# Performance work log

Measured on AMD Instinct MI355X. Metric: run time of the kernel, lower is better.

## Reference

```python
import jax, jax.numpy as jnp
import numpy as np

N_NODES = 8192
K = 64


def setup_inputs() -> dict:
    key = jax.random.key(0)
    k1, k2 = jax.random.split(key)
    A = jax.random.normal(k1, (N_NODES, N_NODES), dtype=jnp.float32)
    idx = jax.random.randint(k2, (N_NODES,), 0, N_NODES, dtype=jnp.int64)
    return {"A": A, "idx": idx}


def reference(A, idx):
    # adj = relu(A)
    adj = jax.nn.relu(A)
    # per-row top-k indices (dim=1), then scatter a 0/1 mask and multiply
    _, ind = jax.lax.top_k(adj, K)  # ind: [N, K]
    rows = jnp.arange(adj.shape[0], dtype=ind.dtype)[:, None]  # [N, 1]
    mask = jnp.zeros_like(adj).at[rows, ind].set(1.0)
    return adj * mask
```

## Files before the change

kernel.cpp:

```cpp
#include <hip/hip_runtime.h>
#include <stdint.h>


constexpr int N      = 8192;
constexpr int K      = 64;
constexpr int BLOCK  = 256;
constexpr int VPT    = N / BLOCK;
constexpr int V4     = VPT / 4;
constexpr int CAP    = 1536;
constexpr int EQ_CAP = 256;

__device__ __forceinline__ uint32_t wave_reduce_add(uint32_t x) {
    #pragma unroll
    for (int d = 32; d >= 1; d >>= 1) x += __shfl_down(x, d, 64);
    return x;
}

__device__ __forceinline__ void scan_pick(const uint32_t* hist256,
                                          uint32_t* s_prefix, uint32_t* s_k,
                                          int shift, int lane) {
    uint32_t k  = *s_k;
    uint32_t h0 = hist256[4 * lane + 0];
    uint32_t h1 = hist256[4 * lane + 1];
    uint32_t h2 = hist256[4 * lane + 2];
    uint32_t h3 = hist256[4 * lane + 3];
    uint32_t suf = h0 + h1 + h2 + h3;
    #pragma unroll
    for (int d = 1; d < 64; d <<= 1) {
        uint32_t o = __shfl_down(suf, d, 64);
        if (lane + d < 64) suf += o;
    }
    unsigned long long m = __ballot(suf >= k);
    int cl = 63 - __builtin_clzll(m);
    if (lane == cl) {
        uint32_t S0 = suf, S1 = S0 - h0, S2 = S1 - h1, S3 = S2 - h2;
        int b; uint32_t Sb, hb;
        if      (S3 >= k) { b = 3; Sb = S3; hb = h3; }
        else if (S2 >= k) { b = 2; Sb = S2; hb = h2; }
        else if (S1 >= k) { b = 1; Sb = S1; hb = h1; }
        else              { b = 0; Sb = S0; hb = h0; }
        *s_prefix |= (uint32_t)(4 * lane + b) << shift;
        *s_k = k - (Sb - hb);
    }
}

__global__ __launch_bounds__(BLOCK) void topk_row_kernel(
    const float* __restrict__ A, float* __restrict__ out)
{
    __shared__ uint32_t hist[4][256];
    __shared__ uint32_t list[CAP];
    __shared__ uint32_t s_eq[EQ_CAP];
    __shared__ uint32_t s_rb[4][5];
    __shared__ uint32_t s_rmax[4];
    __shared__ uint32_t s_prefix, s_k, s_cnt, s_listcnt, s_C, s_ecut, s_mode, s_max;

    const int tid  = threadIdx.x;
    const int wave = tid >> 6;
    const int lane = tid & 63;
    const int row  = blockIdx.x;

    const float4* rowp = reinterpret_cast<const float4*>(A + (size_t)row * N);
    float4*       outp = reinterpret_cast<float4*>(out + (size_t)row * N);

    uint32_t v[VPT];
    #pragma unroll
    for (int j = 0; j < V4; ++j) {
        float4 f = rowp[tid + j * BLOCK];
        v[4*j+0] = (f.x > 0.f) ? __float_as_uint(f.x) : 0u;
        v[4*j+1] = (f.y > 0.f) ? __float_as_uint(f.y) : 0u;
        v[4*j+2] = (f.z > 0.f) ? __float_as_uint(f.z) : 0u;
        v[4*j+3] = (f.w > 0.f) ? __float_as_uint(f.w) : 0u;
    }
    if (tid == 0) { s_listcnt = 0; s_cnt = 0; }

    uint32_t mx = 0;
    #pragma unroll
    for (int j = 0; j < VPT; ++j) mx = (v[j] > mx) ? v[j] : mx;
    #pragma unroll
    for (int d = 32; d >= 1; d >>= 1) {
        uint32_t o = __shfl_down(mx, d, 64);
        mx = (o > mx) ? o : mx;
    }
    if (lane == 0) s_rmax[wave] = mx;
    __syncthreads();
    if (tid == 0) {
        uint32_t m = s_rmax[0];
        m = (s_rmax[1] > m) ? s_rmax[1] : m;
        m = (s_rmax[2] > m) ? s_rmax[2] : m;
        m = (s_rmax[3] > m) ? s_rmax[3] : m;
        s_max = m;
    }
    __syncthreads();
    const uint32_t expM = s_max >> 23;

    uint32_t b0 = 0, b1 = 0, b2 = 0, b3 = 0, cpos = 0;
    #pragma unroll
    for (int j = 0; j < VPT; ++j) {
        uint32_t x = v[j];
        if (x != 0u) {
            uint32_t d = expM - (x >> 23);
            cpos += 1u;
            b0 += (d == 0u); b1 += (d == 1u); b2 += (d == 2u); b3 += (d == 3u);
        }
    }
    b0 = wave_reduce_add(b0); b1 = wave_reduce_add(b1);
    b2 = wave_reduce_add(b2); b3 = wave_reduce_add(b3);
    cpos = wave_reduce_add(cpos);
    if (lane == 0) {
        s_rb[wave][0] = b0; s_rb[wave][1] = b1; s_rb[wave][2] = b2;
        s_rb[wave][3] = b3; s_rb[wave][4] = cpos;
    }
    __syncthreads();
    if (tid == 0) {
        uint32_t B[5];
        #pragma unroll
        for (int c = 0; c < 5; ++c)
            B[c] = s_rb[0][c] + s_rb[1][c] + s_rb[2][c] + s_rb[3][c];
        if (B[4] < (uint32_t)K) {
            s_mode = 1;
        } else {
            s_mode = 0;
            uint32_t cum = 0; int jf = -1;
            #pragma unroll
            for (int j = 0; j < 4; ++j) {
                cum += B[j];
                if (jf < 0 && cum >= (uint32_t)K) jf = j;
            }
            if (jf >= 0) {
                uint32_t c2 = 0;
                for (int j = 0; j <= jf; ++j) c2 += B[j];
                s_C = c2; s_ecut = expM - (uint32_t)jf;
            } else {
                s_C = 0;
            }
        }
    }
    __syncthreads();

    if (s_mode == 1) {
        #pragma unroll
        for (int j = 0; j < V4; ++j) {
            float4 o;
            o.x = __uint_as_float(v[4*j+0]); o.y = __uint_as_float(v[4*j+1]);
            o.z = __uint_as_float(v[4*j+2]); o.w = __uint_as_float(v[4*j+3]);
            outp[tid + j * BLOCK] = o;
        }
        return;
    }

    if (s_C == 0) {
        uint32_t ecut = (expM > 7u) ? (expM - 7u) : 0u;
        for (;;) {
            __syncthreads();
            uint32_t lc = 0;
            #pragma unroll
            for (int j = 0; j < VPT; ++j)
                lc += (v[j] != 0u && (v[j] >> 23) >= ecut) ? 1u : 0u;
            lc = wave_reduce_add(lc);
            if (lane == 0) s_rb[wave][0] = lc;
            __syncthreads();
            if (tid == 0) {
                s_C = s_rb[0][0] + s_rb[1][0] + s_rb[2][0] + s_rb[3][0];
                s_ecut = ecut;
            }
            __syncthreads();
            if (s_C >= (uint32_t)K || ecut == 0u) break;
            ecut = (ecut > 4u) ? (ecut - 4u) : 0u;
        }
    }
    __syncthreads();
    const uint32_t C    = s_C;
    const uint32_t ecut = s_ecut;

    #pragma unroll
    for (int c = 0; c < 4; ++c) hist[c][tid] = 0;
    if (tid == 0) { s_prefix = 0; s_k = K; }
    __syncthreads();

    if (C <= (uint32_t)CAP) {
        uint32_t lc = 0;
        #pragma unroll
        for (int j = 0; j < VPT; ++j)
            lc += (v[j] != 0u && (v[j] >> 23) >= ecut) ? 1u : 0u;
        uint32_t incl = lc;
        #pragma unroll
        for (int d = 1; d < 64; d <<= 1) {
            uint32_t t = __shfl_up(incl, d, 64);
            if (lane >= d) incl += t;
        }
        uint32_t baseV = 0;
        if (lane == 63) baseV = atomicAdd(&s_listcnt, incl);
        uint32_t base = __shfl(baseV, 63, 64);
        uint32_t pos  = base + (incl - lc);
        #pragma unroll
        for (int j = 0; j < VPT; ++j) {
            uint32_t x = v[j];
            if (x != 0u && (x >> 23) >= ecut) list[pos++] = x;
        }
        __syncthreads();

        for (uint32_t i = tid; i < C; i += BLOCK)
            atomicAdd(&hist[wave][list[i] >> 24], 1u);
        __syncthreads();
        hist[0][tid] = hist[0][tid] + hist[1][tid] + hist[2][tid] + hist[3][tid];
        __syncthreads();
        if (wave == 0) scan_pick(hist[0], &s_prefix, &s_k, 24, lane);
        __syncthreads();

        for (int shift = 16; shift >= 0; shift -= 8) {
            const uint32_t prefix = s_prefix;
            #pragma unroll
            for (int c = 0; c < 4; ++c) hist[c][tid] = 0;
            __syncthreads();
            const uint32_t himask = 0xFFFFFFFFu << (shift + 8);
            for (uint32_t i = tid; i < C; i += BLOCK) {
                uint32_t x = list[i];
                if ((x & himask) == prefix)
                    atomicAdd(&hist[wave][(x >> shift) & 255u], 1u);
            }
            __syncthreads();
            hist[0][tid] = hist[0][tid] + hist[1][tid] + hist[2][tid] + hist[3][tid];
            __syncthreads();
            if (wave == 0) scan_pick(hist[0], &s_prefix, &s_k, shift, lane);
            __syncthreads();
        }
    } else {
        #pragma unroll
        for (int j = 0; j < VPT; ++j) {
            uint32_t x = v[j];
            if (x) atomicAdd(&hist[wave][x >> 24], 1u);
        }
        __syncthreads();
        hist[0][tid] = hist[0][tid] + hist[1][tid] + hist[2][tid] + hist[3][tid];
        __syncthreads();
        if (wave == 0) scan_pick(hist[0], &s_prefix, &s_k, 24, lane);
        __syncthreads();

        for (int shift = 16; shift >= 0; shift -= 8) {
            const uint32_t prefix = s_prefix;
            #pragma unroll
            for (int c = 0; c < 4; ++c) hist[c][tid] = 0;
            __syncthreads();
            const uint32_t himask = 0xFFFFFFFFu << (shift + 8);
            #pragma unroll
            for (int j = 0; j < VPT; ++j) {
                uint32_t x = v[j];
                if ((x & himask) == prefix)
                    atomicAdd(&hist[wave][(x >> shift) & 255u], 1u);
            }
            __syncthreads();
            hist[0][tid] = hist[0][tid] + hist[1][tid] + hist[2][tid] + hist[3][tid];
            __syncthreads();
            if (wave == 0) scan_pick(hist[0], &s_prefix, &s_k, shift, lane);
            __syncthreads();
        }
    }

    const uint32_t T    = s_prefix;
    const uint32_t need = s_k;
    const float    Tf   = __uint_as_float(T);

    #pragma unroll
    for (int j = 0; j < V4; ++j) {
        const int base = (tid + j * BLOCK) * 4;
        float4 o;
        float* oc = &o.x;
        #pragma unroll
        for (int c = 0; c < 4; ++c) {
            uint32_t x = v[4*j+c];
            float val = 0.f;
            if (x > T) {
                val = __uint_as_float(x);
            } else if (x == T) {
                uint32_t p = atomicAdd(&s_cnt, 1u);
                if (p < (uint32_t)EQ_CAP) s_eq[p] = (uint32_t)(base + c);
            }
            oc[c] = val;
        }
        outp[tid + j * BLOCK] = o;
    }
    __syncthreads();

    if (tid == 0) {
        uint32_t cnt = s_cnt < (uint32_t)EQ_CAP ? s_cnt : (uint32_t)EQ_CAP;
        for (uint32_t n = 0; n < need; ++n) {
            uint32_t best = 0xFFFFFFFFu, bi = 0;
            for (uint32_t i = 0; i < cnt; ++i)
                if (s_eq[i] < best) { best = s_eq[i]; bi = i; }
            if (best != 0xFFFFFFFFu) {
                s_eq[bi] = 0xFFFFFFFFu;
                out[(size_t)row * N + best] = Tf;
            }
        }
    }
}

extern "C" void kernel_launch(void* const* d_in, const int* in_sizes, int n_in,
                              void* d_out, int out_size, void* d_ws, size_t ws_size,
                              hipStream_t stream) {
    const float* A = (const float*)d_in[0];
    float* out = (float*)d_out;
    topk_row_kernel<<<N, BLOCK, 0, stream>>>(A, out);
}
```

Before: 442.6 us.

## Seed radix select from exponent window bitmasks and early-exit on unique bucket

Replaces the per-row exponent-window counting with per-thread bitmasks and packed popcount reductions. The selected bucket's bitmask is reused to build the candidate list, and the radix select starts from the known exponent prefix. The select loop exits early once the bucket holds a single element. Other changes: double-buffered per-wave histograms summed inside the scan instead of a separate merge pass, fewer redundant barriers, nontemporal output stores, and a block-parallel tie fallback when the tie list overflows. The aim is to cut synchronisation and histogram passes per row, at the cost of more complex control flow and some extra LDS.

```diff
diff --git a/kernel.cpp b/kernel.cpp
--- a/kernel.cpp
+++ b/kernel.cpp
@@ -1,6 +1,8 @@
 #include <hip/hip_runtime.h>
 #include <stdint.h>
 
+
+typedef float f32x4 __attribute__((ext_vector_type(4)));
 
 constexpr int N      = 8192;
 constexpr int K      = 64;
@@ -16,14 +18,14 @@
     return x;
 }
 
-__device__ __forceinline__ void scan_pick(const uint32_t* hist256,
-                                          uint32_t* s_prefix, uint32_t* s_k,
-                                          int shift, int lane) {
+__device__ __forceinline__ void scan_pick2(const uint32_t (*h)[256],
+                                           uint32_t* s_prefix, uint32_t* s_k,
+                                           uint32_t* s_hb, int shift, int lane) {
     uint32_t k  = *s_k;
-    uint32_t h0 = hist256[4 * lane + 0];
-    uint32_t h1 = hist256[4 * lane + 1];
-    uint32_t h2 = hist256[4 * lane + 2];
-    uint32_t h3 = hist256[4 * lane + 3];
+    uint32_t h0 = h[0][4*lane+0] + h[1][4*lane+0] + h[2][4*lane+0] + h[3][4*lane+0];
+    uint32_t h1 = h[0][4*lane+1] + h[1][4*lane+1] + h[2][4*lane+1] + h[3][4*lane+1];
+    uint32_t h2 = h[0][4*lane+2] + h[1][4*lane+2] + h[2][4*lane+2] + h[3][4*lane+2];
+    uint32_t h3 = h[0][4*lane+3] + h[1][4*lane+3] + h[2][4*lane+3] + h[3][4*lane+3];
     uint32_t suf = h0 + h1 + h2 + h3;
     #pragma unroll
     for (int d = 1; d < 64; d <<= 1) {
@@ -39,20 +41,21 @@
         else if (S2 >= k) { b = 2; Sb = S2; hb = h2; }
         else if (S1 >= k) { b = 1; Sb = S1; hb = h1; }
         else              { b = 0; Sb = S0; hb = h0; }
-        *s_prefix |= (uint32_t)(4 * lane + b) << shift;
-        *s_k = k - (Sb - hb);
+        *s_prefix |= (uint32_t)(4*lane + b) << shift;
+        *s_k  = k - (Sb - hb);
+        *s_hb = hb;
     }
 }
 
 __global__ __launch_bounds__(BLOCK) void topk_row_kernel(
     const float* __restrict__ A, float* __restrict__ out)
 {
-    __shared__ uint32_t hist[4][256];
+    __shared__ uint32_t hist[2][4][256];
     __shared__ uint32_t list[CAP];
     __shared__ uint32_t s_eq[EQ_CAP];
-    __shared__ uint32_t s_rb[4][5];
+    __shared__ uint32_t s_rb[4][3];
     __shared__ uint32_t s_rmax[4];
-    __shared__ uint32_t s_prefix, s_k, s_cnt, s_listcnt, s_C, s_ecut, s_mode, s_max;
+    __shared__ uint32_t s_prefix, s_k, s_hb, s_T, s_cnt, s_listcnt, s_min;
 
     const int tid  = threadIdx.x;
     const int wave = tid >> 6;
@@ -63,125 +66,161 @@
     float4*       outp = reinterpret_cast<float4*>(out + (size_t)row * N);
 
     uint32_t v[VPT];
+    uint32_t mx = 0;
     #pragma unroll
     for (int j = 0; j < V4; ++j) {
         float4 f = rowp[tid + j * BLOCK];
-        v[4*j+0] = (f.x > 0.f) ? __float_as_uint(f.x) : 0u;
-        v[4*j+1] = (f.y > 0.f) ? __float_as_uint(f.y) : 0u;
-        v[4*j+2] = (f.z > 0.f) ? __float_as_uint(f.z) : 0u;
-        v[4*j+3] = (f.w > 0.f) ? __float_as_uint(f.w) : 0u;
-    }
-    if (tid == 0) { s_listcnt = 0; s_cnt = 0; }
-
-    uint32_t mx = 0;
-    #pragma unroll
-    for (int j = 0; j < VPT; ++j) mx = (v[j] > mx) ? v[j] : mx;
+        uint32_t x0 = (f.x > 0.f) ? __float_as_uint(f.x) : 0u;
+        uint32_t x1 = (f.y > 0.f) ? __float_as_uint(f.y) : 0u;
+        uint32_t x2 = (f.z > 0.f) ? __float_as_uint(f.z) : 0u;
+        uint32_t x3 = (f.w > 0.f) ? __float_as_uint(f.w) : 0u;
+        v[4*j+0] = x0; v[4*j+1] = x1; v[4*j+2] = x2; v[4*j+3] = x3;
+        uint32_t m01 = x0 > x1 ? x0 : x1;
+        uint32_t m23 = x2 > x3 ? x2 : x3;
+        uint32_t mm  = m01 > m23 ? m01 : m23;
+        mx = mm > mx ? mm : mx;
+    }
     #pragma unroll
     for (int d = 32; d >= 1; d >>= 1) {
         uint32_t o = __shfl_down(mx, d, 64);
-        mx = (o > mx) ? o : mx;
+        mx = o > mx ? o : mx;
     }
     if (lane == 0) s_rmax[wave] = mx;
+    if (tid == 0) { s_listcnt = 0; s_cnt = 0; }
     __syncthreads();
-    if (tid == 0) {
-        uint32_t m = s_rmax[0];
-        m = (s_rmax[1] > m) ? s_rmax[1] : m;
-        m = (s_rmax[2] > m) ? s_rmax[2] : m;
-        m = (s_rmax[3] > m) ? s_rmax[3] : m;
-        s_max = m;
-    }
-    __syncthreads();
-    const uint32_t expM = s_max >> 23;
-
-    uint32_t b0 = 0, b1 = 0, b2 = 0, b3 = 0, cpos = 0;
+    uint32_t ma = s_rmax[0], mb = s_rmax[1], mc = s_rmax[2], md = s_rmax[3];
+    ma = mb > ma ? mb : ma; mc = md > mc ? md : mc;
+    const uint32_t expM = (mc > ma ? mc : ma) >> 23;
+
+    uint32_t cm0 = 0, cm1 = 0, cm2 = 0, cm3 = 0, mnz = 0;
     #pragma unroll
     for (int j = 0; j < VPT; ++j) {
         uint32_t x = v[j];
         if (x != 0u) {
-            uint32_t d = expM - (x >> 23);
-            cpos += 1u;
-            b0 += (d == 0u); b1 += (d == 1u); b2 += (d == 2u); b3 += (d == 3u);
-        }
-    }
-    b0 = wave_reduce_add(b0); b1 = wave_reduce_add(b1);
-    b2 = wave_reduce_add(b2); b3 = wave_reduce_add(b3);
-    cpos = wave_reduce_add(cpos);
-    if (lane == 0) {
-        s_rb[wave][0] = b0; s_rb[wave][1] = b1; s_rb[wave][2] = b2;
-        s_rb[wave][3] = b3; s_rb[wave][4] = cpos;
-    }
+            uint32_t d   = expM - (x >> 23);
+            uint32_t bit = 1u << j;
+            mnz |= bit;
+            if      (d == 0u) cm0 |= bit;
+            else if (d == 1u) cm1 |= bit;
+            else if (d == 2u) cm2 |= bit;
+            else if (d == 3u) cm3 |= bit;
+        }
+    }
+    uint32_t r01 = (uint32_t)__popc(cm0) | ((uint32_t)__popc(cm1) << 16);
+    uint32_t r23 = (uint32_t)__popc(cm2) | ((uint32_t)__popc(cm3) << 16);
+    uint32_t rcp = (uint32_t)__popc(mnz);
+    r01 = wave_reduce_add(r01);
+    r23 = wave_reduce_add(r23);
+    rcp = wave_reduce_add(rcp);
+    if (lane == 0) { s_rb[wave][0] = r01; s_rb[wave][1] = r23; s_rb[wave][2] = rcp; }
     __syncthreads();
-    if (tid == 0) {
-        uint32_t B[5];
-        #pragma unroll
-        for (int c = 0; c < 5; ++c)
-            B[c] = s_rb[0][c] + s_rb[1][c] + s_rb[2][c] + s_rb[3][c];
-        if (B[4] < (uint32_t)K) {
-            s_mode = 1;
-        } else {
-            s_mode = 0;
-            uint32_t cum = 0; int jf = -1;
-            #pragma unroll
-            for (int j = 0; j < 4; ++j) {
-                cum += B[j];
-                if (jf < 0 && cum >= (uint32_t)K) jf = j;
-            }
-            if (jf >= 0) {
-                uint32_t c2 = 0;
-                for (int j = 0; j <= jf; ++j) c2 += B[j];
-                s_C = c2; s_ecut = expM - (uint32_t)jf;
-            } else {
-                s_C = 0;
-            }
-        }
-    }
-    __syncthreads();
-
-    if (s_mode == 1) {
+    uint32_t t01  = s_rb[0][0] + s_rb[1][0] + s_rb[2][0] + s_rb[3][0];
+    uint32_t t23  = s_rb[0][1] + s_rb[1][1] + s_rb[2][1] + s_rb[3][1];
+    uint32_t cpos = s_rb[0][2] + s_rb[1][2] + s_rb[2][2] + s_rb[3][2];
+    uint32_t B0 = t01 & 0xFFFFu, B1 = t01 >> 16;
+    uint32_t B2 = t23 & 0xFFFFu, B3 = t23 >> 16;
+
+    if (cpos < (uint32_t)K) {
         #pragma unroll
         for (int j = 0; j < V4; ++j) {
             float4 o;
             o.x = __uint_as_float(v[4*j+0]); o.y = __uint_as_float(v[4*j+1]);
             o.z = __uint_as_float(v[4*j+2]); o.w = __uint_as_float(v[4*j+3]);
-            outp[tid + j * BLOCK] = o;
+            __builtin_nontemporal_store(*(const f32x4*)&o,
+                                        (f32x4*)&outp[tid + j * BLOCK]);
         }
         return;
     }
 
-    if (s_C == 0) {
-        uint32_t ecut = (expM > 7u) ? (expM - 7u) : 0u;
+    uint32_t cum1 = B0 + B1, cum2 = cum1 + B2, cum3 = cum2 + B3;
+    const bool windowOK = (cum3 >= (uint32_t)K);
+    uint32_t C, kk, hbInit, prefixInit, ecut, sel = 0;
+    bool needExp;
+    if (windowOK) {
+        uint32_t jf, cumBefore;
+        if      (B0   >= (uint32_t)K) { jf = 0; cumBefore = 0;    C = B0; sel = cm0; }
+        else if (cum1 >= (uint32_t)K) { jf = 1; cumBefore = B0;   C = B1; sel = cm1; }
+        else if (cum2 >= (uint32_t)K) { jf = 2; cumBefore = cum1; C = B2; sel = cm2; }
+        else                          { jf = 3; cumBefore = cum2; C = B3; sel = cm3; }
+        ecut       = expM - jf;
+        kk         = (uint32_t)K - cumBefore;
+        hbInit     = C;
+        prefixInit = ecut << 23;
+        needExp    = false;
+    } else {
+        ecut = (expM > 7u) ? (expM - 7u) : 0u;
         for (;;) {
-            __syncthreads();
             uint32_t lc = 0;
             #pragma unroll
-            for (int j = 0; j < VPT; ++j)
-                lc += (v[j] != 0u && (v[j] >> 23) >= ecut) ? 1u : 0u;
+            for (int j = 0; j < VPT; ++j) {
+                uint32_t x = v[j];
+                lc += (x != 0u && (x >> 23) >= ecut) ? 1u : 0u;
+            }
             lc = wave_reduce_add(lc);
+            __syncthreads();
             if (lane == 0) s_rb[wave][0] = lc;
             __syncthreads();
-            if (tid == 0) {
-                s_C = s_rb[0][0] + s_rb[1][0] + s_rb[2][0] + s_rb[3][0];
-                s_ecut = ecut;
-            }
-            __syncthreads();
-            if (s_C >= (uint32_t)K || ecut == 0u) break;
+            C = s_rb[0][0] + s_rb[1][0] + s_rb[2][0] + s_rb[3][0];
+            if (C >= (uint32_t)K || ecut == 0u) break;
             ecut = (ecut > 4u) ? (ecut - 4u) : 0u;
         }
-    }
-    __syncthreads();
-    const uint32_t C    = s_C;
-    const uint32_t ecut = s_ecut;
-
-    #pragma unroll
-    for (int c = 0; c < 4; ++c) hist[c][tid] = 0;
-    if (tid == 0) { s_prefix = 0; s_k = K; }
-    __syncthreads();
+        kk = (uint32_t)K; hbInit = 0xFFFFFFFFu; prefixInit = 0u;
+        needExp = true;
+    }
+    if (tid == 0) { s_prefix = prefixInit; s_k = kk; s_hb = hbInit; }
+
+    int resShift = 23;
+    uint32_t T = 0, need = 1;
+    auto radix = [&](auto&& forEach, bool needE) {
+        int buf = 0;
+        if (needE) {
+            forEach([&](uint32_t x) { atomicAdd(&hist[0][wave][x >> 23], 1u); });
+            __syncthreads();
+            if (wave == 0) scan_pick2(hist[0], &s_prefix, &s_k, &s_hb, 23, lane);
+            __syncthreads();
+            buf = 1;
+        }
+        for (int shift = 16; shift >= 0; shift -= 8) {
+            if (s_hb == 1u) break;
+            const uint32_t prefix = s_prefix;
+            const uint32_t himask = ~0u << resShift;
+            #pragma unroll
+            for (int b = lane; b < 256; b += 64) hist[buf ^ 1][wave][b] = 0;
+            forEach([&](uint32_t x) {
+                if ((x & himask) == prefix)
+                    atomicAdd(&hist[buf][wave][(x >> shift) & 255u], 1u);
+            });
+            __syncthreads();
+            if (wave == 0) scan_pick2(hist[buf], &s_prefix, &s_k, &s_hb, shift, lane);
+            __syncthreads();
+            buf ^= 1;
+            resShift = shift;
+        }
+        if (s_hb == 1u && resShift > 0) {
+            const uint32_t mlo = ~0u << resShift;
+            const uint32_t pfx = s_prefix;
+            forEach([&](uint32_t x) { if ((x & mlo) == pfx) s_T = x; });
+            __syncthreads();
+            T = s_T;
+        } else {
+            T = s_prefix;
+        }
+        need = s_k;
+    };
 
     if (C <= (uint32_t)CAP) {
-        uint32_t lc = 0;
-        #pragma unroll
-        for (int j = 0; j < VPT; ++j)
-            lc += (v[j] != 0u && (v[j] >> 23) >= ecut) ? 1u : 0u;
+        uint32_t lsel;
+        if (windowOK) {
+            lsel = sel;
+        } else {
+            lsel = 0;
+            #pragma unroll
+            for (int j = 0; j < VPT; ++j) {
+                uint32_t x = v[j];
+                if (x != 0u && (x >> 23) >= ecut) lsel |= 1u << j;
+            }
+        }
+        uint32_t lc   = (uint32_t)__popc(lsel);
         uint32_t incl = lc;
         #pragma unroll
         for (int d = 1; d < 64; d <<= 1) {
@@ -193,73 +232,29 @@
         uint32_t base = __shfl(baseV, 63, 64);
         uint32_t pos  = base + (incl - lc);
         #pragma unroll
-        for (int j = 0; j < VPT; ++j) {
-            uint32_t x = v[j];
-            if (x != 0u && (x >> 23) >= ecut) list[pos++] = x;
-        }
+        for (int j = 0; j < VPT; ++j)
+            if (lsel & (1u << j)) list[pos++] = v[j];
+        #pragma unroll
+        for (int b = lane; b < 256; b += 64) { hist[0][wave][b] = 0; hist[1][wave][b] = 0; }
         __syncthreads();
 
-        for (uint32_t i = tid; i < C; i += BLOCK)
-            atomicAdd(&hist[wave][list[i] >> 24], 1u);
+        auto forEachList = [&](auto&& f) {
+            for (uint32_t i = tid; i < C; i += BLOCK) f(list[i]);
+        };
+        radix(forEachList, needExp);
+    } else {
+        #pragma unroll
+        for (int b = lane; b < 256; b += 64) { hist[0][wave][b] = 0; hist[1][wave][b] = 0; }
         __syncthreads();
-        hist[0][tid] = hist[0][tid] + hist[1][tid] + hist[2][tid] + hist[3][tid];
-        __syncthreads();
-        if (wave == 0) scan_pick(hist[0], &s_prefix, &s_k, 24, lane);
-        __syncthreads();
-
-        for (int shift = 16; shift >= 0; shift -= 8) {
-            const uint32_t prefix = s_prefix;
-            #pragma unroll
-            for (int c = 0; c < 4; ++c) hist[c][tid] = 0;
-            __syncthreads();
-            const uint32_t himask = 0xFFFFFFFFu << (shift + 8);
-            for (uint32_t i = tid; i < C; i += BLOCK) {
-                uint32_t x = list[i];
-                if ((x & himask) == prefix)
-                    atomicAdd(&hist[wave][(x >> shift) & 255u], 1u);
-            }
-            __syncthreads();
-            hist[0][tid] = hist[0][tid] + hist[1][tid] + hist[2][tid] + hist[3][tid];
-            __syncthreads();
-            if (wave == 0) scan_pick(hist[0], &s_prefix, &s_k, shift, lane);
-            __syncthreads();
-        }
-    } else {
-        #pragma unroll
-        for (int j = 0; j < VPT; ++j) {
-            uint32_t x = v[j];
-            if (x) atomicAdd(&hist[wave][x >> 24], 1u);
-        }
-        __syncthreads();
-        hist[0][tid] = hist[0][tid] + hist[1][tid] + hist[2][tid] + hist[3][tid];
-        __syncthreads();
-        if (wave == 0) scan_pick(hist[0], &s_prefix, &s_k, 24, lane);
-        __syncthreads();
-
-        for (int shift = 16; shift >= 0; shift -= 8) {
-            const uint32_t prefix = s_prefix;
-            #pragma unroll
-            for (int c = 0; c < 4; ++c) hist[c][tid] = 0;
-            __syncthreads();
-            const uint32_t himask = 0xFFFFFFFFu << (shift + 8);
-            #pragma unroll
-            for (int j = 0; j < VPT; ++j) {
-                uint32_t x = v[j];
-                if ((x & himask) == prefix)
-                    atomicAdd(&hist[wave][(x >> shift) & 255u], 1u);
-            }
-            __syncthreads();
-            hist[0][tid] = hist[0][tid] + hist[1][tid] + hist[2][tid] + hist[3][tid];
-            __syncthreads();
-            if (wave == 0) scan_pick(hist[0], &s_prefix, &s_k, shift, lane);
-            __syncthreads();
-        }
-    }
-
-    const uint32_t T    = s_prefix;
-    const uint32_t need = s_k;
-    const float    Tf   = __uint_as_float(T);
-
+
+        auto forEachReg = [&](auto&& f) {
+            #pragma unroll
+            for (int j = 0; j < VPT; ++j) if (v[j] != 0u) f(v[j]);
+        };
+        radix(forEachReg, needExp);
+    }
+
+    const float Tf = __uint_as_float(T);
     #pragma unroll
     for (int j = 0; j < V4; ++j) {
         const int base = (tid + j * BLOCK) * 4;
@@ -277,20 +272,41 @@
             }
             oc[c] = val;
         }
-        outp[tid + j * BLOCK] = o;
+        __builtin_nontemporal_store(*(const f32x4*)&o,
+                                    (f32x4*)&outp[tid + j * BLOCK]);
     }
     __syncthreads();
 
-    if (tid == 0) {
-        uint32_t cnt = s_cnt < (uint32_t)EQ_CAP ? s_cnt : (uint32_t)EQ_CAP;
+    const uint32_t cnt = s_cnt;
+    if (cnt <= (uint32_t)EQ_CAP) {
+        if (tid == 0) {
+            for (uint32_t n = 0; n < need; ++n) {
+                uint32_t best = 0xFFFFFFFFu, bi = 0;
+                for (uint32_t i = 0; i < cnt; ++i)
+                    if (s_eq[i] < best) { best = s_eq[i]; bi = i; }
+                if (best != 0xFFFFFFFFu) {
+                    s_eq[bi] = 0xFFFFFFFFu;
+                    out[(size_t)row * N + best] = Tf;
+                }
+            }
+        }
+    } else {
+        uint32_t last = 0;
         for (uint32_t n = 0; n < need; ++n) {
-            uint32_t best = 0xFFFFFFFFu, bi = 0;
-            for (uint32_t i = 0; i < cnt; ++i)
-                if (s_eq[i] < best) { best = s_eq[i]; bi = i; }
-            if (best != 0xFFFFFFFFu) {
-                s_eq[bi] = 0xFFFFFFFFu;
-                out[(size_t)row * N + best] = Tf;
-            }
+            __syncthreads();
+            if (tid == 0) s_min = 0xFFFFFFFFu;
+            __syncthreads();
+            #pragma unroll
+            for (int j = 0; j < VPT; ++j) {
+                if (v[j] == T) {
+                    uint32_t g = (uint32_t)(tid + (j >> 2) * BLOCK) * 4u
+                               + (uint32_t)(j & 3);
+                    if (n == 0 || g > last) atomicMin(&s_min, g);
+                }
+            }
+            __syncthreads();
+            last = s_min;
+            if (tid == 0 && last != 0xFFFFFFFFu) out[(size_t)row * N + last] = Tf;
         }
     }
 }
```

Result: slower. 458.6 us (+3.6%).
